# Kernel tuning notes

Measured on AMD Instinct MI355X. Metric: run time of the kernel, lower is better.

The kernel has to match this reference:

```python
import jax, jax.numpy as jnp
import numpy as np


def setup_inputs() -> dict:
    key = jax.random.key(0)
    k1, k2, k3, k4, k5 = jax.random.split(key, 5)
    B, S, T = 256, 512, 64
    emissions = jax.random.normal(k1, (B, S, T), dtype=jnp.float32)
    tags = jax.random.randint(k2, (B, S), 0, T, dtype=jnp.int64)
    mask = jnp.ones((B, S), dtype=jnp.int32)
    init_range = 0.1
    start_transitions = jax.random.uniform(k3, (T,), minval=-init_range, maxval=init_range, dtype=jnp.float32)
    end_transitions = jax.random.uniform(k4, (T,), minval=-init_range, maxval=init_range, dtype=jnp.float32)
    transitions = jax.random.uniform(k5, (T, T), minval=-init_range, maxval=init_range, dtype=jnp.float32)
    return {"emissions": emissions, "tags": tags, "mask": mask,
            "start_transitions": start_transitions,
            "end_transitions": end_transitions,
            "transitions": transitions}


def _crf_nll_mean(emissions, tags, mask, start_transitions, end_transitions, transitions):
    # batch_first -> time-major: [S, B, T], [S, B]
    em = jnp.transpose(emissions, (1, 0, 2))
    tg = jnp.transpose(tags, (1, 0))
    mk = jnp.transpose(mask, (1, 0))
    maskf = mk.astype(em.dtype)                      # [S, B]
    S, B, T = em.shape
    batch_idx = jnp.arange(B)

    # ---- numerator: score of the gold path (fully vectorized) ----
    emit = jnp.take_along_axis(em, tg[:, :, None], axis=2)[..., 0]   # [S, B]
    trans_sc = transitions[tg[:-1], tg[1:]]                          # [S-1, B]
    score_num = start_transitions[tg[0]] + emit[0]
    score_num = score_num + jnp.sum((trans_sc + emit[1:]) * maskf[1:], axis=0)
    seq_ends = jnp.sum(mk, axis=0) - 1                               # [B]
    last_tags = tg[seq_ends, batch_idx]
    score_num = score_num + end_transitions[last_tags]

    # ---- denominator: log-partition via logsumexp scan ----
    init = start_transitions + em[0]                                 # [B, T]

    def step(score, xs):
        em_i, m_i = xs                                               # [B,T], [B]
        # [B, T_prev, T_next]
        next_score = score[:, :, None] + transitions[None, :, :] + em_i[:, None, :]
        next_score = jax.nn.logsumexp(next_score, axis=1)
        score = jnp.where(m_i[:, None] != 0, next_score, score)
        return score, None

    final, _ = jax.lax.scan(step, init, (em[1:], mk[1:]))
    denom = jax.nn.logsumexp(final + end_transitions, axis=1)        # [B]

    llh = denom - score_num                                          # [B]
    return jnp.mean(llh)                                             # reduction='mean'


def reference(emissions, tags, mask, start_transitions, end_transitions, transitions):
    return _crf_nll_mean(emissions, tags, mask, start_transitions, end_transitions, transitions)
```

## Files before the change

### kernel.cpp

```cpp
#include <hip/hip_runtime.h>

#define BATCH 256
#define SEQ   512
#define NT    64
#define PCH   8
#define CLEN  64
#define PITCH 68

typedef __attribute__((ext_vector_type(8)))  short bf16x8;
typedef __attribute__((ext_vector_type(16))) float f32x16;
typedef __attribute__((ext_vector_type(4)))  float f32x4;

static __device__ __forceinline__ unsigned pk_bf16(float lo, float hi) {
    return (__float_as_uint(hi) & 0xffff0000u) | (__float_as_uint(lo) >> 16);
}
static __device__ __forceinline__ short bf16_trunc(float v) {
    return (short)(__float_as_uint(v) >> 16);
}

__global__ __launch_bounds__(64, 2) void crf_chunk_kernel(
    const float* __restrict__ emissions,
    const float* __restrict__ trans,
    unsigned short* __restrict__ mats,
    float* __restrict__ ws_head)
{
    __shared__ __align__(16) unsigned char smem[CLEN * NT * 4];
    float (*w_lds)[NT] = (float (*)[NT])smem;
    unsigned short* ldsT = (unsigned short*)smem;

    const int c    = blockIdx.x;
    const int b    = blockIdx.y;
    const int lane = threadIdx.x;
    const int h    = lane >> 5;
    const int ml   = lane & 31;

    if (c == 0 && b == 0 && lane == 0) {
        ws_head[0] = 0.f;
        ((unsigned*)ws_head)[1] = 0u;
    }

    const int s0 = c * CLEN;
    int L = (SEQ - 1) - s0; if (L > CLEN) L = CLEN;

    const float* em_b = emissions + (size_t)b * SEQ * NT;
    for (int s = 0; s < L; ++s)
        w_lds[s][lane] = __expf(em_b[(size_t)(s0 + 1 + s) * NT + lane]);

    bf16x8 Af[2][4];
#pragma unroll
    for (int mt = 0; mt < 2; ++mt) {
        int m = mt * 32 + ml;
#pragma unroll
        for (int kk = 0; kk < 4; ++kk) {
            bf16x8 f;
#pragma unroll
            for (int j = 0; j < 8; ++j) {
                int r = 32 * (kk >> 1) + 16 * (kk & 1) + (j & 3) + 8 * (j >> 2) + 4 * h;
                f[j] = bf16_trunc(__expf(trans[r * NT + m]) * 0.0078125f);
            }
            Af[mt][kk] = f;
        }
    }

    union BU { unsigned u[4]; bf16x8 v; };
    BU Bv[4][2];
#pragma unroll
    for (int kk = 0; kk < 4; ++kk)
#pragma unroll
        for (int nt = 0; nt < 2; ++nt) {
            int n = nt * 32 + ml;
#pragma unroll
            for (int d = 0; d < 4; ++d) {
                int j0 = 2 * d;
                int r0 = 32 * (kk >> 1) + 16 * (kk & 1) + (j0 & 3) + 8 * (j0 >> 2) + 4 * h;
                unsigned lo = (r0     == n) ? 0x3f80u : 0u;
                unsigned hi = (r0 + 1 == n) ? 0x3f80u : 0u;
                Bv[kk][nt].u[d] = lo | (hi << 16);
            }
        }

    __threadfence_block();

    const f32x16 zf = {};

    for (int s = 0; s < L; ++s) {
        f32x4 wq[4][2];
#pragma unroll
        for (int kk = 0; kk < 4; ++kk) {
            int base = 32 * (kk >> 1) + 16 * (kk & 1) + 4 * h;
            wq[kk][0] = *(const f32x4*)&w_lds[s][base];
            wq[kk][1] = *(const f32x4*)&w_lds[s][base + 8];
        }

        f32x16 acc[2][2];
#pragma unroll
        for (int mt = 0; mt < 2; ++mt)
#pragma unroll
            for (int nt = 0; nt < 2; ++nt) {
                f32x16 a = __builtin_amdgcn_mfma_f32_32x32x16_bf16(Af[mt][0], Bv[0][nt].v, zf, 0, 0, 0);
                a = __builtin_amdgcn_mfma_f32_32x32x16_bf16(Af[mt][1], Bv[1][nt].v, a, 0, 0, 0);
                a = __builtin_amdgcn_mfma_f32_32x32x16_bf16(Af[mt][2], Bv[2][nt].v, a, 0, 0, 0);
                a = __builtin_amdgcn_mfma_f32_32x32x16_bf16(Af[mt][3], Bv[3][nt].v, a, 0, 0, 0);
                acc[mt][nt] = a;
            }

#pragma unroll
        for (int kk = 0; kk < 4; ++kk) {
            const int mt_s = kk >> 1, qo = 8 * (kk & 1);
#pragma unroll
            for (int nt = 0; nt < 2; ++nt) {
#pragma unroll
                for (int d = 0; d < 4; ++d) {
                    int j0 = 2 * d;
                    float v0 = acc[mt_s][nt][qo + j0]     * wq[kk][j0 >> 2][j0 & 3];
                    float v1 = acc[mt_s][nt][qo + j0 + 1] * wq[kk][(j0 + 1) >> 2][(j0 + 1) & 3];
                    Bv[kk][nt].u[d] = pk_bf16(v0, v1);
                }
            }
        }
    }

    __threadfence_block();
#pragma unroll
    for (int kk = 0; kk < 4; ++kk)
#pragma unroll
        for (int nt = 0; nt < 2; ++nt) {
            int n = nt * 32 + ml;
#pragma unroll
            for (int d = 0; d < 4; ++d) {
                int j0 = 2 * d;
                int r0 = 32 * (kk >> 1) + 16 * (kk & 1) + (j0 & 3) + 8 * (j0 >> 2) + 4 * h;
                *(unsigned*)&ldsT[n * PITCH + r0] = Bv[kk][nt].u[d];
            }
        }
    __threadfence_block();

    unsigned short* outp = mats + ((size_t)(b * PCH + c)) * 4096;
    for (int it = 0; it < 8; ++it) {
        int o = it * 512 + lane * 8;
        int n = o >> 6, k = o & 63;
        const uint2* p = (const uint2*)(ldsT + n * PITCH + k);
        uint2 x = p[0], y = p[1];
        uint4 q4; q4.x = x.x; q4.y = x.y; q4.z = y.x; q4.w = y.y;
        *(uint4*)(outp + o) = q4;
    }
}

__global__ __launch_bounds__(256) void crf_combine_kernel(
    const float* __restrict__ emissions,
    const int*   __restrict__ tags,
    const int*   __restrict__ mask,
    const float* __restrict__ start_tr,
    const float* __restrict__ end_tr,
    const float* __restrict__ trans,
    const unsigned short* __restrict__ mats,
    float* __restrict__ ws_head,
    float* __restrict__ out)
{
    __shared__ __align__(16) float r_lds[NT];
    __shared__ float score_lds;

    const int b    = blockIdx.x;
    const int tid  = threadIdx.x;
    const int j    = tid & 63;
    const int wave = tid >> 6;

    const float* em_b = emissions + (size_t)b * SEQ * NT;
    const int*   tg_b = tags + b * SEQ;
    const int*   mk_b = mask + b * SEQ;
    const unsigned short* mb = mats + (size_t)b * PCH * 4096;

    float denom = 0.f;

    if (wave >= 2) {
        const uint4* p = (const uint4*)mb;
        unsigned acc = 0;
        for (int i = (wave - 2) * 64 + j; i < PCH * 512; i += 128) {
            uint4 q = p[i];
            acc += q.x + q.y + q.z + q.w;
        }
        if (acc == 0xdeadbeefu) ws_head[2] = -1.f;
    } else if (wave == 1) {
        float part = 0.f;
        int mcount = 0;
        for (int s = j; s < SEQ; s += 64) {
            int m = mk_b[s];
            mcount += m;
            int t = tg_b[s];
            if (s == 0) {
                part += start_tr[t] + em_b[t];
            } else {
                int tp = tg_b[s - 1];
                float v = trans[tp * NT + t] + em_b[s * NT + t];
                part += m ? v : 0.f;
            }
        }
#pragma unroll
        for (int d = 32; d; d >>= 1) {
            part   += __shfl_xor(part, d);
            mcount += __shfl_xor(mcount, d);
        }
        if (j == 0) score_lds = part + end_tr[tg_b[mcount - 1]];
    } else {
        float r = __expf(end_tr[j]);
        r_lds[j] = r;
        __threadfence_block();
        int X = 0;

        uint4 cur[8], nxt[8];
#pragma unroll
        for (int u = 0; u < 8; ++u)
            cur[u] = *(const uint4*)(mb + (size_t)(PCH - 1) * 4096 + j * 64 + u * 8);

        for (int c = PCH - 1; c >= 0; --c) {
            if (c > 0) {
#pragma unroll
                for (int u = 0; u < 8; ++u)
                    nxt[u] = *(const uint4*)(mb + (size_t)(c - 1) * 4096 + j * 64 + u * 8);
            }
            float a0 = 0.f, a1 = 0.f, a2 = 0.f, a3 = 0.f;
#pragma unroll
            for (int u = 0; u < 8; ++u) {
                uint4 q = cur[u];
                f32x4 ra = *(const f32x4*)&r_lds[u * 8];
                f32x4 rb = *(const f32x4*)&r_lds[u * 8 + 4];
                a0 = fmaf(ra[0], __uint_as_float(q.x << 16),         a0);
                a1 = fmaf(ra[1], __uint_as_float(q.x & 0xffff0000u), a1);
                a2 = fmaf(ra[2], __uint_as_float(q.y << 16),         a2);
                a3 = fmaf(ra[3], __uint_as_float(q.y & 0xffff0000u), a3);
                a0 = fmaf(rb[0], __uint_as_float(q.z << 16),         a0);
                a1 = fmaf(rb[1], __uint_as_float(q.z & 0xffff0000u), a1);
                a2 = fmaf(rb[2], __uint_as_float(q.w << 16),         a2);
                a3 = fmaf(rb[3], __uint_as_float(q.w & 0xffff0000u), a3);
            }
            float rn = (a0 + a1) + (a2 + a3);
            unsigned eb = (__builtin_amdgcn_readfirstlane((int)__float_as_uint(rn)) >> 23) & 0xffu;
            r = rn * __uint_as_float((254u - eb) << 23);
            X += (int)eb - 127;
            r_lds[j] = r;
            __threadfence_block();
#pragma unroll
            for (int u = 0; u < 8; ++u) cur[u] = nxt[u];
        }

        float u0 = __expf(start_tr[j] + em_b[j]);
        float v = r * u0;
#pragma unroll
        for (int d = 32; d; d >>= 1) v += __shfl_xor(v, d);
        denom = __logf(v) + (float)(X + 7 * (SEQ - 1)) * 0.6931471805599453f;
    }

    __syncthreads();

    if (wave == 0 && j == 0) {
        float llh = denom - score_lds;
        atomicAdd(&ws_head[0], llh * (1.0f / BATCH));
        __threadfence();
        unsigned old = atomicAdd((unsigned*)ws_head + 1, 1u);
        if (old == BATCH - 1) {
            __threadfence();
            out[0] = atomicAdd(&ws_head[0], 0.0f);
        }
    }
}

extern "C" void kernel_launch(void* const* d_in, const int* in_sizes, int n_in,
                              void* d_out, int out_size, void* d_ws, size_t ws_size,
                              hipStream_t stream) {
    const float* emissions = (const float*)d_in[0];
    const int*   tags      = (const int*)d_in[1];
    const int*   mask      = (const int*)d_in[2];
    const float* start_tr  = (const float*)d_in[3];
    const float* end_tr    = (const float*)d_in[4];
    const float* trans     = (const float*)d_in[5];

    float* ws_head = (float*)d_ws;
    unsigned short* mats = (unsigned short*)((char*)d_ws + 4096);

    crf_chunk_kernel<<<dim3(PCH, BATCH), 64, 0, stream>>>(emissions, trans, mats, ws_head);
    crf_combine_kernel<<<BATCH, 256, 0, stream>>>(emissions, tags, mask,
                                                  start_tr, end_tr, trans, mats,
                                                  ws_head, (float*)d_out);
}
```

Baseline: 154.5 us.

## Split sequence into more chunks and move gold-path scoring into chunk kernel

Raises the chunk count from 8 to 12 (chunk length 43), which shortens the serial per-chunk matrix-product chain and gives the first kernel more blocks. The gold-path numerator is now computed as per-chunk partial sums inside the chunk kernel, so the combine kernel shrinks to a single wave. That wave reduces the partials and runs the backward chain over the chunk matrices with a three-deep load prefetch. Bf16 packing switches from truncation to round-to-nearest, and a dummy checksum wave that read the matrices is removed. In exchange, the combine step now has 12 serial matrix-vector steps instead of 8, and rounding adds a little ALU work per chunk step.

```diff
diff --git a/kernel.cpp b/kernel.cpp
--- a/kernel.cpp
+++ b/kernel.cpp
@@ -1,28 +1,39 @@
 #include <hip/hip_runtime.h>
+#include <hip/hip_bf16.h>
 
 #define BATCH 256
 #define SEQ   512
 #define NT    64
-#define PCH   8
-#define CLEN  64
+#define PCH   12
+#define CLEN  43
 #define PITCH 68
 
 typedef __attribute__((ext_vector_type(8)))  short bf16x8;
 typedef __attribute__((ext_vector_type(16))) float f32x16;
 typedef __attribute__((ext_vector_type(4)))  float f32x4;
 
-static __device__ __forceinline__ unsigned pk_bf16(float lo, float hi) {
-    return (__float_as_uint(hi) & 0xffff0000u) | (__float_as_uint(lo) >> 16);
-}
+#define MEMBAR() __asm__ __volatile__("" ::: "memory")
+
 static __device__ __forceinline__ short bf16_trunc(float v) {
     return (short)(__float_as_uint(v) >> 16);
 }
+static __device__ __forceinline__ unsigned pack_bf16_rn(float lo, float hi) {
+    float2 f; f.x = lo; f.y = hi;
+    __hip_bfloat162 h = __float22bfloat162_rn(f);
+    unsigned u; __builtin_memcpy(&u, &h, 4);
+    return u;
+}
 
 __global__ __launch_bounds__(64, 2) void crf_chunk_kernel(
     const float* __restrict__ emissions,
+    const int*   __restrict__ tags,
+    const int*   __restrict__ mask,
+    const float* __restrict__ start_tr,
     const float* __restrict__ trans,
     unsigned short* __restrict__ mats,
-    float* __restrict__ ws_head)
+    float* __restrict__ ws_head,
+    float* __restrict__ score_part,
+    int*   __restrict__ mcnt_part)
 {
     __shared__ __align__(16) unsigned char smem[CLEN * NT * 4];
     float (*w_lds)[NT] = (float (*)[NT])smem;
@@ -43,8 +54,37 @@
     int L = (SEQ - 1) - s0; if (L > CLEN) L = CLEN;
 
     const float* em_b = emissions + (size_t)b * SEQ * NT;
+    const int*   tg_b = tags + b * SEQ;
+    const int*   mk_b = mask + b * SEQ;
+
     for (int s = 0; s < L; ++s)
         w_lds[s][lane] = __expf(em_b[(size_t)(s0 + 1 + s) * NT + lane]);
+
+    float np = 0.f;
+    int   mc = 0;
+    if (lane < L) {
+        int s  = s0 + 1 + lane;
+        int m  = mk_b[s];
+        mc = m;
+        int t  = tg_b[s];
+        int tp = tg_b[s - 1];
+        float v = trans[tp * NT + t] + em_b[(size_t)s * NT + t];
+        np = m ? v : 0.f;
+    }
+    if (c == 0 && lane == 0) {
+        int t0 = tg_b[0];
+        np += start_tr[t0] + em_b[t0];
+        mc += mk_b[0];
+    }
+#pragma unroll
+    for (int d = 32; d; d >>= 1) {
+        np += __shfl_xor(np, d);
+        mc += __shfl_xor(mc, d);
+    }
+    if (lane == 0) {
+        score_part[b * PCH + c] = np;
+        mcnt_part[b * PCH + c]  = mc;
+    }
 
     bf16x8 Af[2][4];
 #pragma unroll
@@ -79,7 +119,7 @@
             }
         }
 
-    __threadfence_block();
+    __syncthreads();
 
     const f32x16 zf = {};
 
@@ -112,9 +152,9 @@
 #pragma unroll
                 for (int d = 0; d < 4; ++d) {
                     int j0 = 2 * d;
-                    float v0 = acc[mt_s][nt][qo + j0]     * wq[kk][j0 >> 2][j0 & 3];
-                    float v1 = acc[mt_s][nt][qo + j0 + 1] * wq[kk][(j0 + 1) >> 2][(j0 + 1) & 3];
-                    Bv[kk][nt].u[d] = pk_bf16(v0, v1);
+                    float v0 = acc[mt_s][nt][qo + j0]     * wq[kk][d >> 1][2 * (d & 1)];
+                    float v1 = acc[mt_s][nt][qo + j0 + 1] * wq[kk][d >> 1][2 * (d & 1) + 1];
+                    Bv[kk][nt].u[d] = pack_bf16_rn(v0, v1);
                 }
             }
         }
@@ -146,114 +186,91 @@
     }
 }
 
-__global__ __launch_bounds__(256) void crf_combine_kernel(
+__global__ __launch_bounds__(64) void crf_combine_kernel(
     const float* __restrict__ emissions,
     const int*   __restrict__ tags,
-    const int*   __restrict__ mask,
     const float* __restrict__ start_tr,
     const float* __restrict__ end_tr,
-    const float* __restrict__ trans,
     const unsigned short* __restrict__ mats,
+    const float* __restrict__ score_part,
+    const int*   __restrict__ mcnt_part,
     float* __restrict__ ws_head,
     float* __restrict__ out)
 {
     __shared__ __align__(16) float r_lds[NT];
-    __shared__ float score_lds;
-
-    const int b    = blockIdx.x;
-    const int tid  = threadIdx.x;
-    const int j    = tid & 63;
-    const int wave = tid >> 6;
+
+    const int b = blockIdx.x;
+    const int j = threadIdx.x;
 
     const float* em_b = emissions + (size_t)b * SEQ * NT;
     const int*   tg_b = tags + b * SEQ;
-    const int*   mk_b = mask + b * SEQ;
     const unsigned short* mb = mats + (size_t)b * PCH * 4096;
 
-    float denom = 0.f;
-
-    if (wave >= 2) {
-        const uint4* p = (const uint4*)mb;
-        unsigned acc = 0;
-        for (int i = (wave - 2) * 64 + j; i < PCH * 512; i += 128) {
-            uint4 q = p[i];
-            acc += q.x + q.y + q.z + q.w;
-        }
-        if (acc == 0xdeadbeefu) ws_head[2] = -1.f;
-    } else if (wave == 1) {
-        float part = 0.f;
-        int mcount = 0;
-        for (int s = j; s < SEQ; s += 64) {
-            int m = mk_b[s];
-            mcount += m;
-            int t = tg_b[s];
-            if (s == 0) {
-                part += start_tr[t] + em_b[t];
-            } else {
-                int tp = tg_b[s - 1];
-                float v = trans[tp * NT + t] + em_b[s * NT + t];
-                part += m ? v : 0.f;
-            }
-        }
-#pragma unroll
-        for (int d = 32; d; d >>= 1) {
-            part   += __shfl_xor(part, d);
-            mcount += __shfl_xor(mcount, d);
-        }
-        if (j == 0) score_lds = part + end_tr[tg_b[mcount - 1]];
-    } else {
-        float r = __expf(end_tr[j]);
+    float sp = (j < PCH) ? score_part[b * PCH + j] : 0.f;
+    int   mp = (j < PCH) ? mcnt_part[b * PCH + j] : 0;
+
+    float r = __expf(end_tr[j]);
+    r_lds[j] = r;
+    MEMBAR();
+    int X = 0;
+
+    uint4 buf[3][8];
+#pragma unroll
+    for (int u = 0; u < 8; ++u)
+        buf[0][u] = *(const uint4*)(mb + (size_t)(PCH - 1) * 4096 + j * 64 + u * 8);
+#pragma unroll
+    for (int u = 0; u < 8; ++u)
+        buf[1][u] = *(const uint4*)(mb + (size_t)(PCH - 2) * 4096 + j * 64 + u * 8);
+
+#pragma unroll
+    for (int d = 32; d; d >>= 1) {
+        sp += __shfl_xor(sp, d);
+        mp += __shfl_xor(mp, d);
+    }
+    int last_tag = tg_b[mp - 1];
+    float score_num = sp + end_tr[last_tag];
+
+#pragma unroll
+    for (int c = PCH - 1; c >= 0; --c) {
+        const int slot  = (PCH - 1 - c) % 3;
+        const int nslot = (PCH - 1 - c + 2) % 3;
+        if (c >= 2) {
+#pragma unroll
+            for (int u = 0; u < 8; ++u)
+                buf[nslot][u] = *(const uint4*)(mb + (size_t)(c - 2) * 4096 + j * 64 + u * 8);
+        }
+        float a0 = 0.f, a1 = 0.f, a2 = 0.f, a3 = 0.f;
+#pragma unroll
+        for (int u = 0; u < 8; ++u) {
+            uint4 q = buf[slot][u];
+            f32x4 ra = *(const f32x4*)&r_lds[u * 8];
+            f32x4 rb = *(const f32x4*)&r_lds[u * 8 + 4];
+            a0 = fmaf(ra[0], __uint_as_float(q.x << 16),         a0);
+            a1 = fmaf(ra[1], __uint_as_float(q.x & 0xffff0000u), a1);
+            a2 = fmaf(ra[2], __uint_as_float(q.y << 16),         a2);
+            a3 = fmaf(ra[3], __uint_as_float(q.y & 0xffff0000u), a3);
+            a0 = fmaf(rb[0], __uint_as_float(q.z << 16),         a0);
+            a1 = fmaf(rb[1], __uint_as_float(q.z & 0xffff0000u), a1);
+            a2 = fmaf(rb[2], __uint_as_float(q.w << 16),         a2);
+            a3 = fmaf(rb[3], __uint_as_float(q.w & 0xffff0000u), a3);
+        }
+        float rn = (a0 + a1) + (a2 + a3);
+        unsigned eb = (__builtin_amdgcn_readfirstlane((int)__float_as_uint(rn)) >> 23) & 0xffu;
+        r = rn * __uint_as_float((254u - eb) << 23);
+        X += (int)eb - 127;
+        MEMBAR();
         r_lds[j] = r;
-        __threadfence_block();
-        int X = 0;
-
-        uint4 cur[8], nxt[8];
-#pragma unroll
-        for (int u = 0; u < 8; ++u)
-            cur[u] = *(const uint4*)(mb + (size_t)(PCH - 1) * 4096 + j * 64 + u * 8);
-
-        for (int c = PCH - 1; c >= 0; --c) {
-            if (c > 0) {
-#pragma unroll
-                for (int u = 0; u < 8; ++u)
-                    nxt[u] = *(const uint4*)(mb + (size_t)(c - 1) * 4096 + j * 64 + u * 8);
-            }
-            float a0 = 0.f, a1 = 0.f, a2 = 0.f, a3 = 0.f;
-#pragma unroll
-            for (int u = 0; u < 8; ++u) {
-                uint4 q = cur[u];
-                f32x4 ra = *(const f32x4*)&r_lds[u * 8];
-                f32x4 rb = *(const f32x4*)&r_lds[u * 8 + 4];
-                a0 = fmaf(ra[0], __uint_as_float(q.x << 16),         a0);
-                a1 = fmaf(ra[1], __uint_as_float(q.x & 0xffff0000u), a1);
-                a2 = fmaf(ra[2], __uint_as_float(q.y << 16),         a2);
-                a3 = fmaf(ra[3], __uint_as_float(q.y & 0xffff0000u), a3);
-                a0 = fmaf(rb[0], __uint_as_float(q.z << 16),         a0);
-                a1 = fmaf(rb[1], __uint_as_float(q.z & 0xffff0000u), a1);
-                a2 = fmaf(rb[2], __uint_as_float(q.w << 16),         a2);
-                a3 = fmaf(rb[3], __uint_as_float(q.w & 0xffff0000u), a3);
-            }
-            float rn = (a0 + a1) + (a2 + a3);
-            unsigned eb = (__builtin_amdgcn_readfirstlane((int)__float_as_uint(rn)) >> 23) & 0xffu;
-            r = rn * __uint_as_float((254u - eb) << 23);
-            X += (int)eb - 127;
-            r_lds[j] = r;
-            __threadfence_block();
-#pragma unroll
-            for (int u = 0; u < 8; ++u) cur[u] = nxt[u];
-        }
-
-        float u0 = __expf(start_tr[j] + em_b[j]);
-        float v = r * u0;
-#pragma unroll
-        for (int d = 32; d; d >>= 1) v += __shfl_xor(v, d);
-        denom = __logf(v) + (float)(X + 7 * (SEQ - 1)) * 0.6931471805599453f;
-    }
-
-    __syncthreads();
-
-    if (wave == 0 && j == 0) {
-        float llh = denom - score_lds;
+        MEMBAR();
+    }
+
+    float u0 = __expf(start_tr[j] + em_b[j]);
+    float v = r * u0;
+#pragma unroll
+    for (int d = 32; d; d >>= 1) v += __shfl_xor(v, d);
+
+    if (j == 0) {
+        float denom = __logf(v) + (float)(X + 7 * (SEQ - 1)) * 0.6931471805599453f;
+        float llh = denom - score_num;
         atomicAdd(&ws_head[0], llh * (1.0f / BATCH));
         __threadfence();
         unsigned old = atomicAdd((unsigned*)ws_head + 1, 1u);
@@ -274,11 +291,14 @@
     const float* end_tr    = (const float*)d_in[4];
     const float* trans     = (const float*)d_in[5];
 
-    float* ws_head = (float*)d_ws;
-    unsigned short* mats = (unsigned short*)((char*)d_ws + 4096);
-
-    crf_chunk_kernel<<<dim3(PCH, BATCH), 64, 0, stream>>>(emissions, trans, mats, ws_head);
-    crf_combine_kernel<<<BATCH, 256, 0, stream>>>(emissions, tags, mask,
-                                                  start_tr, end_tr, trans, mats,
-                                                  ws_head, (float*)d_out);
-}
+    float* ws_head    = (float*)d_ws;
+    float* score_part = (float*)((char*)d_ws + 64);
+    int*   mcnt_part  = (int*)((char*)d_ws + 64 + 4 * BATCH * PCH);
+    unsigned short* mats = (unsigned short*)((char*)d_ws + 32768);
+
+    crf_chunk_kernel<<<dim3(PCH, BATCH), 64, 0, stream>>>(
+        emissions, tags, mask, start_tr, trans, mats, ws_head, score_part, mcnt_part);
+    crf_combine_kernel<<<BATCH, 64, 0, stream>>>(
+        emissions, tags, start_tr, end_tr, mats, score_part, mcnt_part,
+        ws_head, (float*)d_out);
+}
```

Result: slower. 166.8 us (+7.9%).
